# Kernel tuning notes

Hardware: AMD Instinct MI355X
Metric: run time of the kernel (lower is better)

Reference implementation:

```python
import jax, jax.numpy as jnp
import numpy as np

U, I, D, NNZ, LAYERS, B = 50000, 50000, 64, 3200000, 3, 4096
N = U + I
L2_REG = 1e-5
EPS = 1e-12


def setup_inputs() -> dict:
    key = jax.random.key(0)
    ks = jax.random.split(key, 12)
    return {
        "users": jax.random.randint(ks[0], (B,), 0, U, dtype=jnp.int64)
        if jax.config.jax_enable_x64 else jax.random.randint(ks[0], (B,), 0, U, dtype=jnp.int32),
        "pos_items": jax.random.randint(ks[1], (B,), 0, N, dtype=jnp.int32),
        "neg_items": jax.random.randint(ks[2], (B,), 0, N, dtype=jnp.int32),
        "rows": jax.random.randint(ks[3], (NNZ,), 0, N, dtype=jnp.int32),
        "cols": jax.random.randint(ks[4], (NNZ,), 0, N, dtype=jnp.int32),
        "vals": jax.random.uniform(ks[5], (NNZ,), dtype=jnp.float32),
        "user_embed": jax.random.normal(ks[6], (U, D), dtype=jnp.float32),
        "item_embed": jax.random.normal(ks[7], (I, D), dtype=jnp.float32),
        "W1": jax.random.normal(ks[8], (LAYERS, D, D), dtype=jnp.float32) * 0.1,
        "b1": jax.random.normal(ks[9], (LAYERS, 1, D), dtype=jnp.float32) * 0.1,
        "W2": jax.random.normal(ks[10], (LAYERS, D, D), dtype=jnp.float32) * 0.1,
        "b2": jax.random.normal(ks[11], (LAYERS, 1, D), dtype=jnp.float32) * 0.1,
    }


def reference(users, pos_items, neg_items, rows, cols, vals,
              user_embed, item_embed, W1, b1, W2, b2):
    # E: [N, D] concatenated user/item embeddings
    E = jnp.concatenate([user_embed, item_embed], axis=0)
    embs = [E]
    for l in range(W1.shape[0]):
        # SpMM: L @ E via edge-wise gather + scatter-add (memory-bound)
        msgs = vals[:, None] * E[cols]                     # [nnz, D]
        L_mul = jax.ops.segment_sum(msgs, rows, num_segments=N)
        A_mul = L_mul + E                                  # A = L + I
        left = A_mul @ W1[l] + b1[l]
        right = (L_mul * E) @ W2[l] + b2[l]
        E = jax.nn.leaky_relu(left + right, negative_slope=0.2)
        # message dropout rate = 0 -> identity
        norm = jnp.maximum(jnp.linalg.norm(E, axis=1, keepdims=True), EPS)
        embs.append(E / norm)
    all_e = jnp.concatenate(embs, axis=1)                  # [N, D*(LAYERS+1)]
    u = all_e[users]
    p = all_e[pos_items]
    n = all_e[neg_items]
    pos_rating = jnp.sum(u * p, axis=1)
    neg_rating = jnp.sum(u * n, axis=1)
    bpr_loss = -jnp.mean(jax.nn.log_sigmoid(pos_rating - neg_rating))
    # faithful to source: neg term is ||n|| (not squared)
    l2norm = (jnp.sum(u ** 2) + jnp.sum(p ** 2) + jnp.sqrt(jnp.sum(n ** 2))) / 2.0
    l2reg = L2_REG * l2norm / u.shape[0]
    return bpr_loss + l2reg
```

## Files before the change

### kernel.cpp

```cpp
#include <hip/hip_runtime.h>
#include <hip/hip_bf16.h>
#include <hip/hip_fp8.h>
#include <math.h>

#define U_CNT 50000
#define I_CNT 50000
#define N_CNT 100000
#define D 64
#define NNZ_CNT 3200000
#define LAYERS 3
#define BATCH 4096
#define L2_REG_F 1e-5f
#define EPS_F 1e-12f

#define NBUCKET 391
#define SC_NBLK 256
#define SC_CHUNK 12500
#define BCNT_N (NBUCKET * SC_NBLK)
#define BCNT_NBLK ((BCNT_N + 255) / 256)

typedef __attribute__((ext_vector_type(8))) short short8;
typedef __attribute__((ext_vector_type(4))) float floatx4;
typedef __attribute__((ext_vector_type(2))) float f32x2v;

__device__ __forceinline__ unsigned short f32_to_bf16(float f) {
    unsigned int u = __float_as_uint(f);
    u += 0x7FFFu + ((u >> 16) & 1u);
    return (unsigned short)(u >> 16);
}
__device__ __forceinline__ float bf16_to_f32(unsigned short h) {
    return __uint_as_float(((unsigned int)h) << 16);
}
__device__ __forceinline__ float bf16_lo(unsigned int u) {
    return __uint_as_float(u << 16);
}
__device__ __forceinline__ float bf16_hi(unsigned int u) {
    return __uint_as_float(u & 0xFFFF0000u);
}
__device__ __forceinline__ unsigned int pack_bf16(float a, float b) {
    return (unsigned int)f32_to_bf16(a) | ((unsigned int)f32_to_bf16(b) << 16);
}

__device__ __forceinline__ unsigned char f32_to_fp8(float v) {
    v = fminf(fmaxf(v, -448.0f), 448.0f);
#if __has_builtin(__builtin_amdgcn_cvt_pk_fp8_f32)
    return (unsigned char)(__builtin_amdgcn_cvt_pk_fp8_f32(v, 0.0f, 0, false) & 0xFF);
#else
    __hip_fp8_e4m3 t(v);
    return (unsigned char)t.__x;
#endif
}
template <bool HI>
__device__ __forceinline__ f32x2v fp8x2_to_f32(unsigned int w) {
#if __has_builtin(__builtin_amdgcn_cvt_pk_f32_fp8)
    return __builtin_amdgcn_cvt_pk_f32_fp8((int)w, HI);
#else
    unsigned int s = HI ? (w >> 16) : (w & 0xFFFFu);
    __hip_fp8_e4m3 a, b;
    a.__x = (unsigned char)(s & 0xFF);
    b.__x = (unsigned char)((s >> 8) & 0xFF);
    f32x2v r;
    r.x = (float)a;
    r.y = (float)b;
    return r;
#endif
}

__global__ void init_E(const float* __restrict__ ue, const float* __restrict__ ie,
                       unsigned short* __restrict__ Ebf, unsigned char* __restrict__ Efp8,
                       float* __restrict__ all_e) {
    int tid = blockIdx.x * blockDim.x + threadIdx.x;
    if (tid >= N_CNT * D) return;
    int row = tid >> 6;
    int d = tid & 63;
    float v = (row < U_CNT) ? ue[tid] : ie[tid - U_CNT * D];
    Ebf[tid] = f32_to_bf16(v);
    Efp8[tid] = f32_to_fp8(v);
    all_e[(size_t)row * 256 + d] = v;
}

__global__ void scan_p1(const int* __restrict__ in, int* __restrict__ bsums, int n) {
    __shared__ int s[256];
    int t = threadIdx.x;
    int i = blockIdx.x * 256 + t;
    int v = (i < n) ? in[i] : 0;
    s[t] = v;
    __syncthreads();
    for (int off = 128; off >= 1; off >>= 1) {
        if (t < off) s[t] += s[t + off];
        __syncthreads();
    }
    if (t == 0) bsums[blockIdx.x] = s[0];
}

__global__ void scan_p2(int* __restrict__ bsums, int nblk) {
    __shared__ int s[512];
    int t = threadIdx.x;
    int v = (t < nblk) ? bsums[t] : 0;
    s[t] = v;
    __syncthreads();
    for (int off = 1; off < 512; off <<= 1) {
        int x = (t >= off) ? s[t - off] : 0;
        __syncthreads();
        s[t] += x;
        __syncthreads();
    }
    if (t < nblk) bsums[t] = s[t] - v;
}

__global__ void scan_p3(const int* __restrict__ in, const int* __restrict__ bsums,
                        int* __restrict__ out, int n) {
    __shared__ int s[256];
    int t = threadIdx.x;
    int i = blockIdx.x * 256 + t;
    int v = (i < n) ? in[i] : 0;
    s[t] = v;
    __syncthreads();
    for (int off = 1; off < 256; off <<= 1) {
        int x = (t >= off) ? s[t - off] : 0;
        __syncthreads();
        s[t] += x;
        __syncthreads();
    }
    if (i < n) out[i] = s[t] - v + bsums[blockIdx.x];
}

__global__ __launch_bounds__(1024) void bucket_hist(const int* __restrict__ rows,
                                                    int* __restrict__ bcnt) {
    __shared__ int h[NBUCKET];
    int blk = blockIdx.x, t = threadIdx.x;
    if (t < NBUCKET) h[t] = 0;
    __syncthreads();
    int s = blk * SC_CHUNK, e = s + SC_CHUNK;
    for (int i = s + t; i < e; i += 1024) atomicAdd(&h[rows[i] >> 8], 1);
    __syncthreads();
    if (t < NBUCKET) bcnt[t * SC_NBLK + blk] = h[t];
}

__global__ __launch_bounds__(1024) void block_scatter(const int* __restrict__ rows,
                                                      const int* __restrict__ cols,
                                                      const float* __restrict__ vals,
                                                      const int* __restrict__ boff,
                                                      float2* __restrict__ bbuf) {
    __shared__ int cur[NBUCKET];
    int blk = blockIdx.x, t = threadIdx.x;
    if (t < NBUCKET) cur[t] = boff[t * SC_NBLK + blk];
    __syncthreads();
    int s = blk * SC_CHUNK, e = s + SC_CHUNK;
    for (int i = s + t; i < e; i += 1024) {
        int r = rows[i];
        int b = r >> 8;
        int p = atomicAdd(&cur[b], 1);
        unsigned int bits = ((unsigned int)(r & 255) << 17) | (unsigned int)cols[i];
        bbuf[p] = make_float2(vals[i], __uint_as_float(bits));
    }
}

__global__ __launch_bounds__(1024) void csr_finalize(const float2* __restrict__ bbuf,
                                                     const int* __restrict__ boff,
                                                     int* __restrict__ row_ptr,
                                                     unsigned int* __restrict__ packed) {
    __shared__ int h[256];
    __shared__ int cur[256];
    int b = blockIdx.x, t = threadIdx.x;
    int s = boff[b * SC_NBLK];
    int e = (b == NBUCKET - 1) ? NNZ_CNT : boff[(b + 1) * SC_NBLK];
    if (t < 256) h[t] = 0;
    __syncthreads();
    for (int i = s + t; i < e; i += 1024)
        atomicAdd(&h[__float_as_uint(bbuf[i].y) >> 17], 1);
    __syncthreads();
    int v = (t < 256) ? h[t] : 0;
    for (int off = 1; off < 256; off <<= 1) {
        int x = (t >= off && t < 256) ? h[t - off] : 0;
        __syncthreads();
        if (t < 256) h[t] += x;
        __syncthreads();
    }
    if (t < 256) {
        int start = s + h[t] - v;
        int row = (b << 8) + t;
        if (row < N_CNT) row_ptr[row] = start;
        cur[t] = start;
        if (b == 0 && t == 0) row_ptr[N_CNT] = NNZ_CNT;
    }
    __syncthreads();
    for (int i = s + t; i < e; i += 1024) {
        float2 rec = bbuf[i];
        unsigned int bits = __float_as_uint(rec.y);
        int p = atomicAdd(&cur[bits >> 17], 1);
        unsigned int q = (unsigned int)(rec.x * 32767.0f + 0.5f);
        packed[p] = (q << 17) | (bits & 0x1FFFFu);
    }
}

__global__ __launch_bounds__(256) void spmm_fp8(const unsigned int* __restrict__ packed,
                                                const int* __restrict__ row_ptr,
                                                const unsigned char* __restrict__ Efp8,
                                                unsigned short* __restrict__ Lm) {
    int wid = (blockIdx.x * blockDim.x + threadIdx.x) >> 6;
    int lane = threadIdx.x & 63;
    if (wid >= N_CNT) return;
    int s = row_ptr[wid];
    int e = row_ptr[wid + 1];
    int eidx = lane >> 3;
    int dlane = lane & 7;
    const unsigned char* Eb = Efp8 + (dlane << 3);
    const float VK = 1.0f / (32767.0f * 131072.0f);
    f32x2v a01 = {0.f, 0.f}, a23 = {0.f, 0.f}, a45 = {0.f, 0.f}, a67 = {0.f, 0.f};
    int nit = (e - s + 7) >> 3;
    int i = s + eidx;
    unsigned int u0 = (i < e) ? packed[i] : 0u;
    unsigned int u1 = (i + 8 < e) ? packed[i + 8] : 0u;
    unsigned int u2 = (i + 16 < e) ? packed[i + 16] : 0u;
    uint2 g0 = *(const uint2*)(Eb + ((size_t)(u0 & 0x1FFFFu) << 6));
    uint2 g1 = *(const uint2*)(Eb + ((size_t)(u1 & 0x1FFFFu) << 6));
#pragma unroll 2
    for (int it = 0; it < nit; ++it) {
        uint2 g2 = *(const uint2*)(Eb + ((size_t)(u2 & 0x1FFFFu) << 6));
        int i3 = i + 24;
        unsigned int u3 = (i3 < e) ? packed[i3] : 0u;
        float vs = (float)u0 * VK;
        f32x2v vv = {vs, vs};
        a01 += vv * fp8x2_to_f32<false>(g0.x);
        a23 += vv * fp8x2_to_f32<true>(g0.x);
        a45 += vv * fp8x2_to_f32<false>(g0.y);
        a67 += vv * fp8x2_to_f32<true>(g0.y);
        u0 = u1; u1 = u2; u2 = u3;
        g0 = g1; g1 = g2;
        i += 8;
    }
    float a0 = a01.x, a1 = a01.y, a2 = a23.x, a3 = a23.y;
    float a4 = a45.x, a5 = a45.y, a6 = a67.x, a7 = a67.y;
#pragma unroll
    for (int off = 32; off >= 8; off >>= 1) {
        a0 += __shfl_xor(a0, off, 64); a1 += __shfl_xor(a1, off, 64);
        a2 += __shfl_xor(a2, off, 64); a3 += __shfl_xor(a3, off, 64);
        a4 += __shfl_xor(a4, off, 64); a5 += __shfl_xor(a5, off, 64);
        a6 += __shfl_xor(a6, off, 64); a7 += __shfl_xor(a7, off, 64);
    }
    if (eidx == 0) {
        unsigned int* dst = (unsigned int*)(Lm + (size_t)wid * D + dlane * 8);
        *(uint4*)dst = make_uint4(pack_bf16(a0, a1), pack_bf16(a2, a3),
                                  pack_bf16(a4, a5), pack_bf16(a6, a7));
    }
}

#define AP 136
__global__ __launch_bounds__(256) void layer_fused_mfma(const unsigned short* __restrict__ Lm,
                                                        unsigned short* __restrict__ Ebf,
                                                        unsigned char* __restrict__ Efp8,
                                                        const float* __restrict__ W1,
                                                        const float* __restrict__ b1,
                                                        const float* __restrict__ W2,
                                                        const float* __restrict__ b2,
                                                        float* __restrict__ all_e, int layer) {
    __shared__ unsigned short sBt[64 * AP];
    __shared__ float sBias[64];
    __shared__ unsigned short sA[4][16 * AP];

    int t = threadIdx.x;
    for (int i = t; i < 4096; i += 256) {
        int k = i >> 6, n = i & 63;
        sBt[n * AP + k] = f32_to_bf16(W1[i]);
        sBt[n * AP + 64 + k] = f32_to_bf16(W2[i]);
    }
    if (t < 64) sBias[t] = b1[t] + b2[t];
    __syncthreads();

    int w = t >> 6, lane = t & 63;
    int quad = lane >> 4, l16 = lane & 15;

    short8 bfrag[4][4];
#pragma unroll
    for (int ks = 0; ks < 4; ks++)
#pragma unroll
        for (int ct = 0; ct < 4; ct++)
            bfrag[ks][ct] = *(const short8*)&sBt[(ct * 16 + l16) * AP + ks * 32 + quad * 8];

    float bias[4];
#pragma unroll
    for (int ct = 0; ct < 4; ct++) bias[ct] = sBias[ct * 16 + l16];

    unsigned short* A = sA[w];
    int col_off = (layer + 1) * 64;
    int nwaves = gridDim.x * 4;

    for (int tile = blockIdx.x * 4 + w; tile < N_CNT / 16; tile += nwaves) {
        int rbase = tile * 16;
#pragma unroll
        for (int p = 0; p < 4; p++) {
            int r = p * 4 + quad;
            int c = l16 * 4;
            uint2 lw = *(const uint2*)(Lm + (size_t)(rbase + r) * 64 + c);
            float l0 = bf16_lo(lw.x), l1 = bf16_hi(lw.x);
            float l2 = bf16_lo(lw.y), l3 = bf16_hi(lw.y);
            ushort4 eh = *(const ushort4*)(Ebf + (size_t)(rbase + r) * 64 + c);
            float e0 = bf16_to_f32(eh.x), e1 = bf16_to_f32(eh.y);
            float e2 = bf16_to_f32(eh.z), e3 = bf16_to_f32(eh.w);
            *(uint2*)&A[r * AP + c] = make_uint2(pack_bf16(l0 + e0, l1 + e1),
                                                pack_bf16(l2 + e2, l3 + e3));
            *(uint2*)&A[r * AP + 64 + c] = make_uint2(pack_bf16(l0 * e0, l1 * e1),
                                                      pack_bf16(l2 * e2, l3 * e3));
        }
        floatx4 acc[4];
#pragma unroll
        for (int ct = 0; ct < 4; ct++) {
            acc[ct][0] = bias[ct]; acc[ct][1] = bias[ct];
            acc[ct][2] = bias[ct]; acc[ct][3] = bias[ct];
        }
#pragma unroll
        for (int ks = 0; ks < 4; ks++) {
            short8 af = *(const short8*)&A[l16 * AP + ks * 32 + quad * 8];
#pragma unroll
            for (int ct = 0; ct < 4; ct++)
                acc[ct] = __builtin_amdgcn_mfma_f32_16x16x32_bf16(af, bfrag[ks][ct], acc[ct], 0, 0, 0);
        }
        float y[4][4];
        float ssq[4] = {0.f, 0.f, 0.f, 0.f};
#pragma unroll
        for (int ct = 0; ct < 4; ct++)
#pragma unroll
            for (int reg = 0; reg < 4; reg++) {
                float v = acc[ct][reg];
                v = (v > 0.f) ? v : 0.2f * v;
                y[ct][reg] = v;
                ssq[reg] += v * v;
            }
#pragma unroll
        for (int reg = 0; reg < 4; reg++) {
            float ss = ssq[reg];
            ss += __shfl_xor(ss, 1, 64);
            ss += __shfl_xor(ss, 2, 64);
            ss += __shfl_xor(ss, 4, 64);
            ss += __shfl_xor(ss, 8, 64);
            ssq[reg] = fmaxf(sqrtf(ss), EPS_F);
        }
#pragma unroll
        for (int reg = 0; reg < 4; reg++) {
            int row = rbase + quad * 4 + reg;
            float inv = 1.0f / ssq[reg];
#pragma unroll
            for (int ct = 0; ct < 4; ct++) {
                int col = ct * 16 + l16;
                float v = y[ct][reg];
                Ebf[(size_t)row * 64 + col] = f32_to_bf16(v);
                all_e[(size_t)row * 256 + col_off + col] = v * inv;
            }
        }
        if (layer < 2) {
            unsigned char* sb = (unsigned char*)A;
#pragma unroll
            for (int reg = 0; reg < 4; reg++) {
                int rl = quad * 4 + reg;
#pragma unroll
                for (int ct = 0; ct < 4; ct++)
                    sb[rl * 64 + ct * 16 + l16] = f32_to_fp8(y[ct][reg]);
            }
            __builtin_amdgcn_wave_barrier();
            uint4 ov = *(const uint4*)(sb + lane * 16);
            *(uint4*)(Efp8 + (size_t)rbase * 64 + lane * 16) = ov;
        }
    }
}

__device__ __forceinline__ float dot4(float4 a, float4 b) {
    return a.x * b.x + a.y * b.y + a.z * b.z + a.w * b.w;
}

__global__ __launch_bounds__(256) void score_kernel(const float* __restrict__ all_e,
                                                    const int* __restrict__ users,
                                                    const int* __restrict__ pos,
                                                    const int* __restrict__ neg,
                                                    float4* __restrict__ partials) {
    int wid = (blockIdx.x * blockDim.x + threadIdx.x) >> 6;
    int lane = threadIdx.x & 63;
    if (wid >= BATCH) return;
    int ui = users[wid];
    int pi = pos[wid];
    int ni = neg[wid];
    const float4* uv4 = (const float4*)(all_e + (size_t)ui * 256);
    const float4* pv4 = (const float4*)(all_e + (size_t)pi * 256);
    const float4* nv4 = (const float4*)(all_e + (size_t)ni * 256);
    float4 uv = uv4[lane];
    float4 pv = pv4[lane];
    float4 nv = nv4[lane];
    float s_up = dot4(uv, pv);
    float s_un = dot4(uv, nv);
    float s_uu = dot4(uv, uv);
    float s_pp = dot4(pv, pv);
    float s_nn = dot4(nv, nv);
#pragma unroll
    for (int off = 32; off >= 1; off >>= 1) {
        s_up += __shfl_xor(s_up, off, 64);
        s_un += __shfl_xor(s_un, off, 64);
        s_uu += __shfl_xor(s_uu, off, 64);
        s_pp += __shfl_xor(s_pp, off, 64);
        s_nn += __shfl_xor(s_nn, off, 64);
    }
    if (lane == 0) {
        float x = s_up - s_un;
        float ls = fminf(x, 0.f) - log1pf(expf(-fabsf(x)));
        partials[wid] = make_float4(-ls, s_uu, s_pp, s_nn);
    }
}

__global__ __launch_bounds__(256) void reduce_finalize(const float4* __restrict__ partials,
                                                       float* __restrict__ out) {
    __shared__ float4 s[256];
    int t = threadIdx.x;
    float4 a = make_float4(0.f, 0.f, 0.f, 0.f);
    for (int i = t; i < BATCH; i += 256) {
        float4 p = partials[i];
        a.x += p.x; a.y += p.y; a.z += p.z; a.w += p.w;
    }
    s[t] = a;
    __syncthreads();
    for (int off = 128; off >= 1; off >>= 1) {
        if (t < off) {
            s[t].x += s[t + off].x;
            s[t].y += s[t + off].y;
            s[t].z += s[t + off].z;
            s[t].w += s[t + off].w;
        }
        __syncthreads();
    }
    if (t == 0) {
        float bpr = s[0].x / (float)BATCH;
        float l2norm = (s[0].y + s[0].z + sqrtf(s[0].w)) * 0.5f;
        out[0] = bpr + L2_REG_F * l2norm / (float)BATCH;
    }
}

extern "C" void kernel_launch(void* const* d_in, const int* in_sizes, int n_in,
                              void* d_out, int out_size, void* d_ws, size_t ws_size,
                              hipStream_t stream) {
    const int* users = (const int*)d_in[0];
    const int* pos_items = (const int*)d_in[1];
    const int* neg_items = (const int*)d_in[2];
    const int* rows = (const int*)d_in[3];
    const int* cols = (const int*)d_in[4];
    const float* vals = (const float*)d_in[5];
    const float* user_embed = (const float*)d_in[6];
    const float* item_embed = (const float*)d_in[7];
    const float* W1 = (const float*)d_in[8];
    const float* b1 = (const float*)d_in[9];
    const float* W2 = (const float*)d_in[10];
    const float* b2 = (const float*)d_in[11];
    float* out = (float*)d_out;

    char* ws = (char*)d_ws;
    size_t off_alle = 0;
    size_t off_packed = off_alle + (size_t)N_CNT * 256 * 4;
    size_t off_Ebf = off_packed + (size_t)NNZ_CNT * 4;
    size_t off_Efp8 = off_Ebf + (size_t)N_CNT * D * 2;
    size_t off_Lm = off_Efp8 + (size_t)N_CNT * D;
    size_t off_rowptr = off_Lm + (size_t)N_CNT * D * 2;
    size_t off_blkB = off_rowptr + 400128;
    size_t off_bcnt = off_blkB + 2048;
    size_t off_part = off_bcnt + 400384;

    float* all_e = (float*)(ws + off_alle);
    float2* bbuf = (float2*)(ws + off_alle);
    unsigned int* packed = (unsigned int*)(ws + off_packed);
    unsigned short* Ebf = (unsigned short*)(ws + off_Ebf);
    unsigned char* Efp8 = (unsigned char*)(ws + off_Efp8);
    unsigned short* Lm = (unsigned short*)(ws + off_Lm);
    int* row_ptr = (int*)(ws + off_rowptr);
    int* blkB = (int*)(ws + off_blkB);
    int* bcnt = (int*)(ws + off_bcnt);
    float4* partials = (float4*)(ws + off_part);

    bucket_hist<<<SC_NBLK, 1024, 0, stream>>>(rows, bcnt);
    scan_p1<<<BCNT_NBLK, 256, 0, stream>>>(bcnt, blkB, BCNT_N);
    scan_p2<<<1, 512, 0, stream>>>(blkB, BCNT_NBLK);
    scan_p3<<<BCNT_NBLK, 256, 0, stream>>>(bcnt, blkB, bcnt, BCNT_N);
    block_scatter<<<SC_NBLK, 1024, 0, stream>>>(rows, cols, vals, bcnt, bbuf);
    csr_finalize<<<NBUCKET, 1024, 0, stream>>>(bbuf, bcnt, row_ptr, packed);

    init_E<<<(N_CNT * D) / 256, 256, 0, stream>>>(user_embed, item_embed, Ebf, Efp8, all_e);

    for (int l = 0; l < LAYERS; l++) {
        spmm_fp8<<<(N_CNT * 64) / 256, 256, 0, stream>>>(packed, row_ptr, Efp8, Lm);
        layer_fused_mfma<<<784, 256, 0, stream>>>(Lm, Ebf, Efp8,
                                                  W1 + (size_t)l * 4096, b1 + (size_t)l * 64,
                                                  W2 + (size_t)l * 4096, b2 + (size_t)l * 64,
                                                  all_e, l);
    }

    score_kernel<<<(BATCH * 64) / 256, 256, 0, stream>>>(all_e, users, pos_items, neg_items,
                                                         partials);
    reduce_finalize<<<1, 256, 0, stream>>>(partials, out);
}
```

Measured before the change: 419.1 us.

## Replace two-level bucket CSR build with direct global-atomic row histogram and scatter

```diff
diff --git a/kernel.cpp b/kernel.cpp
--- a/kernel.cpp
+++ b/kernel.cpp
@@ -13,11 +13,7 @@
 #define L2_REG_F 1e-5f
 #define EPS_F 1e-12f
 
-#define NBUCKET 391
-#define SC_NBLK 256
-#define SC_CHUNK 12500
-#define BCNT_N (NBUCKET * SC_NBLK)
-#define BCNT_NBLK ((BCNT_N + 255) / 256)
+#define RH_NBLK 391
 
 typedef __attribute__((ext_vector_type(8))) short short8;
 typedef __attribute__((ext_vector_type(4))) float floatx4;
@@ -79,6 +75,18 @@
     all_e[(size_t)row * 256 + d] = v;
 }
 
+__global__ void zero_cnt(int* __restrict__ cnt) {
+    int i = blockIdx.x * blockDim.x + threadIdx.x;
+    if (i < N_CNT) cnt[i] = 0;
+}
+
+__global__ __launch_bounds__(256) void row_hist(const int* __restrict__ rows,
+                                                int* __restrict__ cnt) {
+    int stride = gridDim.x * blockDim.x;
+    for (int i = blockIdx.x * blockDim.x + threadIdx.x; i < NNZ_CNT; i += stride)
+        atomicAdd(&cnt[rows[i]], 1);
+}
+
 __global__ void scan_p1(const int* __restrict__ in, int* __restrict__ bsums, int n) {
     __shared__ int s[256];
     int t = threadIdx.x;
@@ -108,8 +116,8 @@
     if (t < nblk) bsums[t] = s[t] - v;
 }
 
-__global__ void scan_p3(const int* __restrict__ in, const int* __restrict__ bsums,
-                        int* __restrict__ out, int n) {
+__global__ void scan_p3_dual(const int* __restrict__ in, const int* __restrict__ bsums,
+                             int* __restrict__ row_ptr, int* __restrict__ cur, int n) {
     __shared__ int s[256];
     int t = threadIdx.x;
     int i = blockIdx.x * 256 + t;
@@ -122,75 +130,25 @@
         s[t] += x;
         __syncthreads();
     }
-    if (i < n) out[i] = s[t] - v + bsums[blockIdx.x];
-}
-
-__global__ __launch_bounds__(1024) void bucket_hist(const int* __restrict__ rows,
-                                                    int* __restrict__ bcnt) {
-    __shared__ int h[NBUCKET];
-    int blk = blockIdx.x, t = threadIdx.x;
-    if (t < NBUCKET) h[t] = 0;
-    __syncthreads();
-    int s = blk * SC_CHUNK, e = s + SC_CHUNK;
-    for (int i = s + t; i < e; i += 1024) atomicAdd(&h[rows[i] >> 8], 1);
-    __syncthreads();
-    if (t < NBUCKET) bcnt[t * SC_NBLK + blk] = h[t];
-}
-
-__global__ __launch_bounds__(1024) void block_scatter(const int* __restrict__ rows,
-                                                      const int* __restrict__ cols,
-                                                      const float* __restrict__ vals,
-                                                      const int* __restrict__ boff,
-                                                      float2* __restrict__ bbuf) {
-    __shared__ int cur[NBUCKET];
-    int blk = blockIdx.x, t = threadIdx.x;
-    if (t < NBUCKET) cur[t] = boff[t * SC_NBLK + blk];
-    __syncthreads();
-    int s = blk * SC_CHUNK, e = s + SC_CHUNK;
-    for (int i = s + t; i < e; i += 1024) {
+    if (i < n) {
+        int excl = s[t] - v + bsums[blockIdx.x];
+        row_ptr[i] = excl;
+        cur[i] = excl;
+    }
+    if (i == 0) row_ptr[N_CNT] = NNZ_CNT;
+}
+
+__global__ __launch_bounds__(256) void row_scatter(const int* __restrict__ rows,
+                                                   const int* __restrict__ cols,
+                                                   const float* __restrict__ vals,
+                                                   int* __restrict__ cur,
+                                                   unsigned int* __restrict__ packed) {
+    int stride = gridDim.x * blockDim.x;
+    for (int i = blockIdx.x * blockDim.x + threadIdx.x; i < NNZ_CNT; i += stride) {
         int r = rows[i];
-        int b = r >> 8;
-        int p = atomicAdd(&cur[b], 1);
-        unsigned int bits = ((unsigned int)(r & 255) << 17) | (unsigned int)cols[i];
-        bbuf[p] = make_float2(vals[i], __uint_as_float(bits));
-    }
-}
-
-__global__ __launch_bounds__(1024) void csr_finalize(const float2* __restrict__ bbuf,
-                                                     const int* __restrict__ boff,
-                                                     int* __restrict__ row_ptr,
-                                                     unsigned int* __restrict__ packed) {
-    __shared__ int h[256];
-    __shared__ int cur[256];
-    int b = blockIdx.x, t = threadIdx.x;
-    int s = boff[b * SC_NBLK];
-    int e = (b == NBUCKET - 1) ? NNZ_CNT : boff[(b + 1) * SC_NBLK];
-    if (t < 256) h[t] = 0;
-    __syncthreads();
-    for (int i = s + t; i < e; i += 1024)
-        atomicAdd(&h[__float_as_uint(bbuf[i].y) >> 17], 1);
-    __syncthreads();
-    int v = (t < 256) ? h[t] : 0;
-    for (int off = 1; off < 256; off <<= 1) {
-        int x = (t >= off && t < 256) ? h[t - off] : 0;
-        __syncthreads();
-        if (t < 256) h[t] += x;
-        __syncthreads();
-    }
-    if (t < 256) {
-        int start = s + h[t] - v;
-        int row = (b << 8) + t;
-        if (row < N_CNT) row_ptr[row] = start;
-        cur[t] = start;
-        if (b == 0 && t == 0) row_ptr[N_CNT] = NNZ_CNT;
-    }
-    __syncthreads();
-    for (int i = s + t; i < e; i += 1024) {
-        float2 rec = bbuf[i];
-        unsigned int bits = __float_as_uint(rec.y);
-        int p = atomicAdd(&cur[bits >> 17], 1);
-        unsigned int q = (unsigned int)(rec.x * 32767.0f + 0.5f);
-        packed[p] = (q << 17) | (bits & 0x1FFFFu);
+        unsigned int q = (unsigned int)(vals[i] * 32767.0f + 0.5f);
+        int p = atomicAdd(&cur[r], 1);
+        packed[p] = (q << 17) | (unsigned int)cols[i];
     }
 }
 
@@ -456,27 +414,28 @@
     size_t off_Efp8 = off_Ebf + (size_t)N_CNT * D * 2;
     size_t off_Lm = off_Efp8 + (size_t)N_CNT * D;
     size_t off_rowptr = off_Lm + (size_t)N_CNT * D * 2;
-    size_t off_blkB = off_rowptr + 400128;
-    size_t off_bcnt = off_blkB + 2048;
-    size_t off_part = off_bcnt + 400384;
+    size_t off_cnt = off_rowptr + 400128;
+    size_t off_cur = off_cnt + 400000;
+    size_t off_blkB = off_cur + 400000;
+    size_t off_part = off_blkB + 2048;
 
     float* all_e = (float*)(ws + off_alle);
-    float2* bbuf = (float2*)(ws + off_alle);
     unsigned int* packed = (unsigned int*)(ws + off_packed);
     unsigned short* Ebf = (unsigned short*)(ws + off_Ebf);
     unsigned char* Efp8 = (unsigned char*)(ws + off_Efp8);
     unsigned short* Lm = (unsigned short*)(ws + off_Lm);
     int* row_ptr = (int*)(ws + off_rowptr);
+    int* cnt = (int*)(ws + off_cnt);
+    int* cur = (int*)(ws + off_cur);
     int* blkB = (int*)(ws + off_blkB);
-    int* bcnt = (int*)(ws + off_bcnt);
     float4* partials = (float4*)(ws + off_part);
 
-    bucket_hist<<<SC_NBLK, 1024, 0, stream>>>(rows, bcnt);
-    scan_p1<<<BCNT_NBLK, 256, 0, stream>>>(bcnt, blkB, BCNT_N);
-    scan_p2<<<1, 512, 0, stream>>>(blkB, BCNT_NBLK);
-    scan_p3<<<BCNT_NBLK, 256, 0, stream>>>(bcnt, blkB, bcnt, BCNT_N);
-    block_scatter<<<SC_NBLK, 1024, 0, stream>>>(rows, cols, vals, bcnt, bbuf);
-    csr_finalize<<<NBUCKET, 1024, 0, stream>>>(bbuf, bcnt, row_ptr, packed);
+    zero_cnt<<<RH_NBLK, 256, 0, stream>>>(cnt);
+    row_hist<<<2048, 256, 0, stream>>>(rows, cnt);
+    scan_p1<<<RH_NBLK, 256, 0, stream>>>(cnt, blkB, N_CNT);
+    scan_p2<<<1, 512, 0, stream>>>(blkB, RH_NBLK);
+    scan_p3_dual<<<RH_NBLK, 256, 0, stream>>>(cnt, blkB, row_ptr, cur, N_CNT);
+    row_scatter<<<2048, 256, 0, stream>>>(rows, cols, vals, cur, packed);
 
     init_E<<<(N_CNT * D) / 256, 256, 0, stream>>>(user_embed, item_embed, Ebf, Efp8, all_e);
 
```

Measured after the change: 640.2 us. 52.8% more time.

## Replace three-pass bucket scan with single-block scan and atomic claims; fuse final reduction

Applied to the files above, without the earlier changes.

```diff
diff --git a/kernel.cpp b/kernel.cpp
--- a/kernel.cpp
+++ b/kernel.cpp
@@ -16,8 +16,6 @@
 #define NBUCKET 391
 #define SC_NBLK 256
 #define SC_CHUNK 12500
-#define BCNT_N (NBUCKET * SC_NBLK)
-#define BCNT_NBLK ((BCNT_N + 255) / 256)
 
 typedef __attribute__((ext_vector_type(8))) short short8;
 typedef __attribute__((ext_vector_type(4))) float floatx4;
@@ -79,52 +77,6 @@
     all_e[(size_t)row * 256 + d] = v;
 }
 
-__global__ void scan_p1(const int* __restrict__ in, int* __restrict__ bsums, int n) {
-    __shared__ int s[256];
-    int t = threadIdx.x;
-    int i = blockIdx.x * 256 + t;
-    int v = (i < n) ? in[i] : 0;
-    s[t] = v;
-    __syncthreads();
-    for (int off = 128; off >= 1; off >>= 1) {
-        if (t < off) s[t] += s[t + off];
-        __syncthreads();
-    }
-    if (t == 0) bsums[blockIdx.x] = s[0];
-}
-
-__global__ void scan_p2(int* __restrict__ bsums, int nblk) {
-    __shared__ int s[512];
-    int t = threadIdx.x;
-    int v = (t < nblk) ? bsums[t] : 0;
-    s[t] = v;
-    __syncthreads();
-    for (int off = 1; off < 512; off <<= 1) {
-        int x = (t >= off) ? s[t - off] : 0;
-        __syncthreads();
-        s[t] += x;
-        __syncthreads();
-    }
-    if (t < nblk) bsums[t] = s[t] - v;
-}
-
-__global__ void scan_p3(const int* __restrict__ in, const int* __restrict__ bsums,
-                        int* __restrict__ out, int n) {
-    __shared__ int s[256];
-    int t = threadIdx.x;
-    int i = blockIdx.x * 256 + t;
-    int v = (i < n) ? in[i] : 0;
-    s[t] = v;
-    __syncthreads();
-    for (int off = 1; off < 256; off <<= 1) {
-        int x = (t >= off) ? s[t - off] : 0;
-        __syncthreads();
-        s[t] += x;
-        __syncthreads();
-    }
-    if (i < n) out[i] = s[t] - v + bsums[blockIdx.x];
-}
-
 __global__ __launch_bounds__(1024) void bucket_hist(const int* __restrict__ rows,
                                                     int* __restrict__ bcnt) {
     __shared__ int h[NBUCKET];
@@ -137,34 +89,79 @@
     if (t < NBUCKET) bcnt[t * SC_NBLK + blk] = h[t];
 }
 
-__global__ __launch_bounds__(1024) void block_scatter(const int* __restrict__ rows,
+__global__ __launch_bounds__(1024) void bucket_scan(const int* __restrict__ bcnt,
+                                                    int* __restrict__ bucket_base,
+                                                    int* __restrict__ cur,
+                                                    float* __restrict__ acc,
+                                                    int* __restrict__ ticket) {
+    __shared__ int tot[512];
+    int t = threadIdx.x;
+    if (t < 512) tot[t] = 0;
+    __syncthreads();
+    if (t < NBUCKET) {
+        const int4* row = (const int4*)(bcnt + t * SC_NBLK);
+        int s = 0;
+#pragma unroll 4
+        for (int k = 0; k < SC_NBLK / 4; k++) {
+            int4 v4 = row[k];
+            s += v4.x + v4.y + v4.z + v4.w;
+        }
+        tot[t] = s;
+    }
+    __syncthreads();
+    int v = (t < 512) ? tot[t] : 0;
+    for (int off = 1; off < 512; off <<= 1) {
+        int x = (t >= off && t < 512) ? tot[t - off] : 0;
+        __syncthreads();
+        if (t < 512) tot[t] += x;
+        __syncthreads();
+    }
+    if (t < NBUCKET) {
+        int base = tot[t] - v;
+        bucket_base[t] = base;
+        cur[t] = base;
+    }
+    if (t == 0) bucket_base[NBUCKET] = NNZ_CNT;
+    if (t < 4) acc[t] = 0.f;
+    if (t == 4) ticket[0] = 0;
+}
+
+__global__ __launch_bounds__(1024) void claim_scatter(const int* __restrict__ rows,
                                                       const int* __restrict__ cols,
                                                       const float* __restrict__ vals,
-                                                      const int* __restrict__ boff,
+                                                      int* __restrict__ cur,
                                                       float2* __restrict__ bbuf) {
-    __shared__ int cur[NBUCKET];
+    __shared__ int h[NBUCKET];
+    __shared__ int curl[NBUCKET];
     int blk = blockIdx.x, t = threadIdx.x;
-    if (t < NBUCKET) cur[t] = boff[t * SC_NBLK + blk];
+    if (t < NBUCKET) h[t] = 0;
     __syncthreads();
     int s = blk * SC_CHUNK, e = s + SC_CHUNK;
+    for (int i = s + t; i < e; i += 1024) atomicAdd(&h[rows[i] >> 8], 1);
+    __syncthreads();
+    if (t < NBUCKET) {
+        int c = h[t];
+        curl[t] = (c > 0) ? atomicAdd(&cur[t], c) : 0;
+    }
+    __syncthreads();
     for (int i = s + t; i < e; i += 1024) {
         int r = rows[i];
         int b = r >> 8;
-        int p = atomicAdd(&cur[b], 1);
+        int p = atomicAdd(&curl[b], 1);
         unsigned int bits = ((unsigned int)(r & 255) << 17) | (unsigned int)cols[i];
         bbuf[p] = make_float2(vals[i], __uint_as_float(bits));
     }
 }
 
 __global__ __launch_bounds__(1024) void csr_finalize(const float2* __restrict__ bbuf,
-                                                     const int* __restrict__ boff,
+                                                     const int* __restrict__ bucket_base,
                                                      int* __restrict__ row_ptr,
                                                      unsigned int* __restrict__ packed) {
     __shared__ int h[256];
     __shared__ int cur[256];
     int b = blockIdx.x, t = threadIdx.x;
-    int s = boff[b * SC_NBLK];
-    int e = (b == NBUCKET - 1) ? NNZ_CNT : boff[(b + 1) * SC_NBLK];
+    int s = bucket_base[b];
+    int e = bucket_base[b + 1];
     if (t < 256) h[t] = 0;
     __syncthreads();
     for (int i = s + t; i < e; i += 1024)
@@ -368,11 +365,13 @@
     return a.x * b.x + a.y * b.y + a.z * b.z + a.w * b.w;
 }
 
-__global__ __launch_bounds__(256) void score_kernel(const float* __restrict__ all_e,
-                                                    const int* __restrict__ users,
-                                                    const int* __restrict__ pos,
-                                                    const int* __restrict__ neg,
-                                                    float4* __restrict__ partials) {
+__global__ __launch_bounds__(256) void score_fused(const float* __restrict__ all_e,
+                                                   const int* __restrict__ users,
+                                                   const int* __restrict__ pos,
+                                                   const int* __restrict__ neg,
+                                                   float* __restrict__ acc,
+                                                   int* __restrict__ ticket,
+                                                   float* __restrict__ out) {
     int wid = (blockIdx.x * blockDim.x + threadIdx.x) >> 6;
     int lane = threadIdx.x & 63;
     if (wid >= BATCH) return;
@@ -401,34 +400,22 @@
     if (lane == 0) {
         float x = s_up - s_un;
         float ls = fminf(x, 0.f) - log1pf(expf(-fabsf(x)));
-        partials[wid] = make_float4(-ls, s_uu, s_pp, s_nn);
-    }
-}
-
-__global__ __launch_bounds__(256) void reduce_finalize(const float4* __restrict__ partials,
-                                                       float* __restrict__ out) {
-    __shared__ float4 s[256];
-    int t = threadIdx.x;
-    float4 a = make_float4(0.f, 0.f, 0.f, 0.f);
-    for (int i = t; i < BATCH; i += 256) {
-        float4 p = partials[i];
-        a.x += p.x; a.y += p.y; a.z += p.z; a.w += p.w;
-    }
-    s[t] = a;
-    __syncthreads();
-    for (int off = 128; off >= 1; off >>= 1) {
-        if (t < off) {
-            s[t].x += s[t + off].x;
-            s[t].y += s[t + off].y;
-            s[t].z += s[t + off].z;
-            s[t].w += s[t + off].w;
-        }
-        __syncthreads();
-    }
-    if (t == 0) {
-        float bpr = s[0].x / (float)BATCH;
-        float l2norm = (s[0].y + s[0].z + sqrtf(s[0].w)) * 0.5f;
-        out[0] = bpr + L2_REG_F * l2norm / (float)BATCH;
+        atomicAdd(&acc[0], -ls);
+        atomicAdd(&acc[1], s_uu);
+        atomicAdd(&acc[2], s_pp);
+        atomicAdd(&acc[3], s_nn);
+        __threadfence();
+        int old = atomicAdd(ticket, 1);
+        if (old == BATCH - 1) {
+            __threadfence();
+            float a0 = atomicAdd(&acc[0], 0.f);
+            float a1 = atomicAdd(&acc[1], 0.f);
+            float a2 = atomicAdd(&acc[2], 0.f);
+            float a3 = atomicAdd(&acc[3], 0.f);
+            float bpr = a0 / (float)BATCH;
+            float l2norm = (a1 + a2 + sqrtf(a3)) * 0.5f;
+            out[0] = bpr + L2_REG_F * l2norm / (float)BATCH;
+        }
     }
 }
 
@@ -456,9 +443,9 @@
     size_t off_Efp8 = off_Ebf + (size_t)N_CNT * D * 2;
     size_t off_Lm = off_Efp8 + (size_t)N_CNT * D;
     size_t off_rowptr = off_Lm + (size_t)N_CNT * D * 2;
-    size_t off_blkB = off_rowptr + 400128;
-    size_t off_bcnt = off_blkB + 2048;
-    size_t off_part = off_bcnt + 400384;
+    size_t off_base = off_rowptr + 400128;
+    size_t off_bcnt = off_base + 2048;
+    size_t off_misc = off_bcnt + 400384;
 
     float* all_e = (float*)(ws + off_alle);
     float2* bbuf = (float2*)(ws + off_alle);
@@ -467,16 +454,16 @@
     unsigned char* Efp8 = (unsigned char*)(ws + off_Efp8);
     unsigned short* Lm = (unsigned short*)(ws + off_Lm);
     int* row_ptr = (int*)(ws + off_rowptr);
-    int* blkB = (int*)(ws + off_blkB);
+    int* bucket_base = (int*)(ws + off_base);
     int* bcnt = (int*)(ws + off_bcnt);
-    float4* partials = (float4*)(ws + off_part);
+    int* cur = (int*)(ws + off_misc);
+    float* acc = (float*)(ws + off_misc + 1600);
+    int* ticket = (int*)(ws + off_misc + 1616);
 
     bucket_hist<<<SC_NBLK, 1024, 0, stream>>>(rows, bcnt);
-    scan_p1<<<BCNT_NBLK, 256, 0, stream>>>(bcnt, blkB, BCNT_N);
-    scan_p2<<<1, 512, 0, stream>>>(blkB, BCNT_NBLK);
-    scan_p3<<<BCNT_NBLK, 256, 0, stream>>>(bcnt, blkB, bcnt, BCNT_N);
-    block_scatter<<<SC_NBLK, 1024, 0, stream>>>(rows, cols, vals, bcnt, bbuf);
-    csr_finalize<<<NBUCKET, 1024, 0, stream>>>(bbuf, bcnt, row_ptr, packed);
+    bucket_scan<<<1, 1024, 0, stream>>>(bcnt, bucket_base, cur, acc, ticket);
+    claim_scatter<<<SC_NBLK, 1024, 0, stream>>>(rows, cols, vals, cur, bbuf);
+    csr_finalize<<<NBUCKET, 1024, 0, stream>>>(bbuf, bucket_base, row_ptr, packed);
 
     init_E<<<(N_CNT * D) / 256, 256, 0, stream>>>(user_embed, item_embed, Ebf, Efp8, all_e);
 
@@ -488,7 +475,6 @@
                                                   all_e, l);
     }
 
-    score_kernel<<<(BATCH * 64) / 256, 256, 0, stream>>>(all_e, users, pos_items, neg_items,
-                                                         partials);
-    reduce_finalize<<<1, 256, 0, stream>>>(partials, out);
-}
+    score_fused<<<(BATCH * 64) / 256, 256, 0, stream>>>(all_e, users, pos_items, neg_items,
+                                                        acc, ticket, out);
+}
```

Measured after the change: 691.8 us. 65.1% more time.
